# Kernel optimization log

Measured on AMD Instinct MI355X. Metric: run time of the kernel, lower is better.

## Reference

```python
import jax, jax.numpy as jnp
import numpy as np

D_IN = 1024
D_OUT = 1024
NUM_HEADS = 16
HEAD_DIM = D_OUT // NUM_HEADS


def setup_inputs() -> dict:
    key = jax.random.key(0)
    ks = jax.random.split(key, 9)
    s = 0.02
    return {
        "x": jax.random.normal(ks[0], (2, 2048, D_IN), dtype=jnp.float32),
        "Wq": jax.random.normal(ks[1], (D_IN, D_OUT), dtype=jnp.float32) * s,
        "bq": jnp.zeros((D_OUT,), dtype=jnp.float32),
        "Wk": jax.random.normal(ks[2], (D_IN, D_OUT), dtype=jnp.float32) * s,
        "bk": jnp.zeros((D_OUT,), dtype=jnp.float32),
        "Wv": jax.random.normal(ks[3], (D_IN, D_OUT), dtype=jnp.float32) * s,
        "bv": jnp.zeros((D_OUT,), dtype=jnp.float32),
        "Wo": jax.random.normal(ks[4], (D_OUT, D_OUT), dtype=jnp.float32) * s,
        "bo": jnp.zeros((D_OUT,), dtype=jnp.float32),
    }


def reference(x, Wq, bq, Wk, bk, Wv, bv, Wo, bo):
    B, S, _ = x.shape
    H, Dh = NUM_HEADS, HEAD_DIM
    q = (x @ Wq + bq).reshape(B, S, H, Dh).transpose(0, 2, 1, 3)  # bhsd
    k = (x @ Wk + bk).reshape(B, S, H, Dh).transpose(0, 2, 1, 3)
    v = (x @ Wv + bv).reshape(B, S, H, Dh).transpose(0, 2, 1, 3)
    scores = jnp.einsum("bhqd,bhkd->bhqk", q, k) * (Dh ** -0.5)
    causal = jnp.tril(jnp.ones((S, S), dtype=bool))
    scores = jnp.where(causal, scores, jnp.float32(-jnp.inf))
    w = jax.nn.softmax(scores, axis=-1)
    ctx = jnp.einsum("bhqk,bhkd->bhqd", w, v)
    ctx = ctx.transpose(0, 2, 1, 3).reshape(B, S, H * Dh)
    return ctx @ Wo + bo
```

## Files before the change

### kernel.cpp

```cpp
#include <hip/hip_runtime.h>
#include <cmath>

#define D_IN 1024
#define D_OUT 1024
#define NUM_HEADS 16
#define HEAD_DIM 64
#define BATCH 2
#define SEQ 2048
#define GK 1024
#define KT 32

typedef __attribute__((ext_vector_type(8))) short short8;
typedef __attribute__((ext_vector_type(4))) short short4v;
typedef __attribute__((ext_vector_type(4))) float float4v;

__device__ __forceinline__ unsigned short f2bf(float f) {
  unsigned int u = __builtin_bit_cast(unsigned int, f);
  unsigned int r = (u + 0x7FFFu + ((u >> 16) & 1u)) >> 16;
  return (unsigned short)r;
}
__device__ __forceinline__ float bf2f(unsigned short h) {
  return __builtin_bit_cast(float, (unsigned int)h << 16);
}

__device__ __forceinline__ void async_copy16(void* lds, const void* g) {
  __builtin_amdgcn_global_load_lds(
      (const __attribute__((address_space(1))) unsigned int*)g,
      (__attribute__((address_space(3))) unsigned int*)lds, 16, 0, 0);
}

#define DPP_F(x, ctrl) __builtin_bit_cast(float,                         \
    __builtin_amdgcn_update_dpp(__builtin_bit_cast(int, (x)),            \
                                __builtin_bit_cast(int, (x)),            \
                                (ctrl), 0xF, 0xF, false))

__device__ __forceinline__ float red16_sum(float x) {
  x += DPP_F(x, 0xB1);
  x += DPP_F(x, 0x4E);
  x += DPP_F(x, 0x124);
  x += DPP_F(x, 0x128);
  return x;
}

__global__ __launch_bounds__(256) void prep(
    const float* __restrict__ x, const float* __restrict__ Wq,
    const float* __restrict__ Wk, const float* __restrict__ Wv,
    const float* __restrict__ Wo, unsigned short* __restrict__ xb,
    unsigned short* __restrict__ wqkv_t, unsigned short* __restrict__ wo_t) {
  const int z = blockIdx.z;
  if (z == 4) {
    const int bid = blockIdx.y * 32 + blockIdx.x;
    const size_t i0 = ((size_t)bid * 256 + threadIdx.x) * 16;
#pragma unroll
    for (int half = 0; half < 2; ++half) {
      const size_t o = i0 + half * 8;
      float4 a = *(const float4*)(x + o);
      float4 b = *(const float4*)(x + o + 4);
      union { unsigned short u[8]; short8 v; } t;
      t.u[0] = f2bf(a.x); t.u[1] = f2bf(a.y); t.u[2] = f2bf(a.z); t.u[3] = f2bf(a.w);
      t.u[4] = f2bf(b.x); t.u[5] = f2bf(b.y); t.u[6] = f2bf(b.z); t.u[7] = f2bf(b.w);
      *(short8*)(xb + o) = t.v;
    }
    return;
  }
  const float* W = (z == 0) ? Wq : (z == 1) ? Wk : (z == 2) ? Wv : Wo;
  unsigned short* out = (z < 3) ? (wqkv_t + (size_t)z * 1024 * 1024) : wo_t;

  __shared__ float T[32][33];
  const int r = threadIdx.x >> 3;
  const int c4 = (threadIdx.x & 7) << 2;
  const int k0 = blockIdx.x * 32, n0 = blockIdx.y * 32;

  float4 v = *(const float4*)(W + (size_t)(k0 + r) * 1024 + n0 + c4);
  T[r][c4 + 0] = v.x; T[r][c4 + 1] = v.y; T[r][c4 + 2] = v.z; T[r][c4 + 3] = v.w;
  __syncthreads();

  union { unsigned short u[4]; short4v v4; } o;
#pragma unroll
  for (int i = 0; i < 4; ++i) o.u[i] = f2bf(T[c4 + i][r]);
  *(short4v*)(out + (size_t)(n0 + r) * 1024 + k0 + c4) = o.v4;
}

__device__ __forceinline__ void gemm_core(
    const unsigned short* __restrict__ A, const unsigned short* __restrict__ Bt,
    unsigned short* As, unsigned short* Bs, int bm, int bn, float4v acc[4][4]) {
  const int tid = threadIdx.x;
  const int wave = tid >> 6, lane = tid & 63;
  const int quad = lane >> 4, l16 = lane & 15;
  const int wr = wave >> 1, wc = wave & 1;
  const int sw = l16 & 7;

  int srow[4], sgc[4];
#pragma unroll
  for (int t = 0; t < 4; ++t) {
    const int c = (wave * 4 + t) * 64 + lane;
    srow[t] = c >> 3;
    sgc[t] = ((c & 7) ^ (srow[t] & 7)) * 8;
  }

  for (int k0 = 0; k0 < GK; k0 += 64) {
    __syncthreads();
#pragma unroll
    for (int t = 0; t < 4; ++t) {
      const int c = (wave * 4 + t) * 64 + lane;
      async_copy16(As + (size_t)c * 8, A + (size_t)(bm + srow[t]) * GK + k0 + sgc[t]);
    }
#pragma unroll
    for (int t = 0; t < 4; ++t) {
      const int c = (wave * 4 + t) * 64 + lane;
      async_copy16(Bs + (size_t)c * 8, Bt + (size_t)(bn + srow[t]) * GK + k0 + sgc[t]);
    }
    __syncthreads();

#pragma unroll
    for (int h = 0; h < 2; ++h) {
      short8 af[4], bf[4];
#pragma unroll
      for (int i = 0; i < 4; ++i) {
        const int row = wr * 64 + i * 16 + l16;
        af[i] = *(const short8*)&As[((size_t)row * 8 + ((h * 4 + quad) ^ sw)) * 8];
      }
#pragma unroll
      for (int j = 0; j < 4; ++j) {
        const int row = wc * 64 + j * 16 + l16;
        bf[j] = *(const short8*)&Bs[((size_t)row * 8 + ((h * 4 + quad) ^ sw)) * 8];
      }
#pragma unroll
      for (int i = 0; i < 4; ++i)
#pragma unroll
        for (int j = 0; j < 4; ++j)
          acc[i][j] = __builtin_amdgcn_mfma_f32_16x16x32_bf16(af[i], bf[j], acc[i][j], 0, 0, 0);
    }
  }
}

__global__ __launch_bounds__(256) void gemm_qkv(
    const unsigned short* __restrict__ A, const unsigned short* __restrict__ Bt,
    const float* __restrict__ bq, const float* __restrict__ bk,
    const float* __restrict__ bv,
    unsigned short* __restrict__ qbuf, unsigned short* __restrict__ kblk,
    unsigned short* __restrict__ vblk) {
  __shared__ unsigned short As[128 * 64];
  __shared__ unsigned short Bs[128 * 64];
  const int wave = threadIdx.x >> 6, lane = threadIdx.x & 63;
  const int quad = lane >> 4, l16 = lane & 15;
  const int wr = wave >> 1, wc = wave & 1;
  const int bm = blockIdx.x * 128, bn = blockIdx.y * 128;

  float4v acc[4][4] = {};
  gemm_core(A, Bt, As, Bs, bm, bn, acc);

#pragma unroll
  for (int j = 0; j < 4; ++j) {
    const int n = bn + wc * 64 + j * 16 + l16;
    const int seg = n >> 10, nn = n & 1023;
    const int h = nn >> 6, d = nn & 63;
    const float bsv = (seg == 0) ? bq[nn] : (seg == 1) ? bk[nn] : bv[nn];
    const float scale = (seg == 0) ? 0.18033688011112043f : 1.0f;
#pragma unroll
    for (int i = 0; i < 4; ++i) {
#pragma unroll
      for (int r = 0; r < 4; ++r) {
        const int m = bm + wr * 64 + i * 16 + quad * 4 + r;
        const int b = m >> 11, s = m & 2047;
        const int bh = b * NUM_HEADS + h;
        const unsigned short hv = f2bf((acc[i][j][r] + bsv) * scale);
        if (seg == 0) {
          qbuf[((size_t)bh * SEQ + s) * HEAD_DIM + d] = hv;
        } else if (seg == 1) {
          kblk[((size_t)bh * 64 + (s >> 5)) * 2048 +
               (size_t)(((((s >> 4) & 1) * 2 + (d >> 5)) * 64 +
                         ((d >> 3) & 3) * 16 + (s & 15)) * 8 + (d & 7))] = hv;
        } else {
          vblk[((size_t)bh * 64 + (s >> 5)) * 2048 +
               (size_t)(((d >> 4) * 64 + ((s >> 3) & 3) * 16 + (d & 15)) * 8 +
                        (s & 7))] = hv;
        }
      }
    }
  }
}

__global__ __launch_bounds__(256) void gemm_out(
    const unsigned short* __restrict__ A, const unsigned short* __restrict__ Bt,
    const float* __restrict__ bo, float* __restrict__ out) {
  __shared__ unsigned short As[128 * 64];
  __shared__ unsigned short Bs[128 * 64];
  const int wave = threadIdx.x >> 6, lane = threadIdx.x & 63;
  const int quad = lane >> 4, l16 = lane & 15;
  const int wr = wave >> 1, wc = wave & 1;
  const int bm = blockIdx.x * 128, bn = blockIdx.y * 128;

  float4v acc[4][4] = {};
  gemm_core(A, Bt, As, Bs, bm, bn, acc);

#pragma unroll
  for (int j = 0; j < 4; ++j) {
    const int n = bn + wc * 64 + j * 16 + l16;
    const float bsv = bo[n];
#pragma unroll
    for (int i = 0; i < 4; ++i) {
#pragma unroll
      for (int r = 0; r < 4; ++r) {
        const int m = bm + wr * 64 + i * 16 + quad * 4 + r;
        out[(size_t)m * D_OUT + n] = acc[i][j][r] + bsv;
      }
    }
  }
}

#define OBS 72

__global__ __launch_bounds__(256) void attn_kernel(
    const unsigned short* __restrict__ qf, const unsigned short* __restrict__ kblk,
    const unsigned short* __restrict__ vblk, unsigned short* __restrict__ ctx) {
  __shared__ unsigned short PL[4 * 32 * 40];
  __shared__ unsigned short OB[4 * 32 * OBS];
  __shared__ float LL[4 * 32];

  const int id = blockIdx.x;
  const int bh = id & 31;
  const int qblk = 63 - (id >> 5);
  const int qw0 = qblk * 32;
  const int tid = threadIdx.x;
  const int w = tid >> 6;
  const int lane = tid & 63;
  const int quad = lane >> 4;
  const int l16 = lane & 15;

  const int nt = qblk + 1;
  const int qch = (nt + 3) >> 2;
  const int t0 = w * qch;
  const int t1 = min(nt, t0 + qch);

  const size_t bh_base = (size_t)bh * SEQ * HEAD_DIM;
  const unsigned short* kb = kblk + bh_base;
  const unsigned short* vb = vblk + bh_base;

  short8 aq[2][2];
#pragma unroll
  for (int qt = 0; qt < 2; ++qt) {
    const unsigned short* qrow =
        qf + bh_base + (size_t)(qw0 + qt * 16 + l16) * HEAD_DIM + quad * 8;
    aq[qt][0] = *(const short8*)qrow;
    aq[qt][1] = *(const short8*)(qrow + 32);
  }

  float4v O[2][4] = {};
  float l_part[2][4] = {};
  unsigned short* PLw = PL + w * (32 * 40);

  if (t0 < t1) {
    short8 kA[4], vA[4], kB[4], vB[4];

    auto load = [&](int kt, short8 kd[4], short8 vd[4]) {
      const size_t base = (size_t)kt * 2048 + lane * 8;
#pragma unroll
      for (int f = 0; f < 4; ++f) kd[f] = *(const short8*)(kb + base + f * 512);
#pragma unroll
      for (int f = 0; f < 4; ++f) vd[f] = *(const short8*)(vb + base + f * 512);
    };

    auto step = [&](int kt, const short8 kd[4], const short8 vd[4], bool masked) {
      const int k0 = kt * KT;
      float4v cs[2][2];
#pragma unroll
      for (int qt = 0; qt < 2; ++qt)
#pragma unroll
        for (int g = 0; g < 2; ++g) {
          float4v c = {0.f, 0.f, 0.f, 0.f};
          c = __builtin_amdgcn_mfma_f32_16x16x32_bf16(aq[qt][0], kd[2 * g], c, 0, 0, 0);
          c = __builtin_amdgcn_mfma_f32_16x16x32_bf16(aq[qt][1], kd[2 * g + 1], c, 0, 0, 0);
          cs[qt][g] = c;
        }

#pragma unroll
      for (int qt = 0; qt < 2; ++qt)
#pragma unroll
        for (int g = 0; g < 2; ++g)
#pragma unroll
          for (int r = 0; r < 4; ++r) {
            float s = cs[qt][g][r];
            if (masked) {
              const int key = k0 + g * 16 + l16;
              const int qg = qw0 + qt * 16 + quad * 4 + r;
              s = (key <= qg) ? s : -1e30f;
            }
            const float p = __builtin_exp2f(s);
            l_part[qt][r] += p;
            const unsigned int pu = __builtin_bit_cast(unsigned int, p);
            PLw[(qt * 16 + quad * 4 + r) * 40 + (g * 2 + (l16 >> 3)) * 8 + (l16 & 7)] =
                (unsigned short)(pu >> 16);
          }

#pragma unroll
      for (int qt = 0; qt < 2; ++qt) {
        const short8 pA = *(const short8*)&PLw[(qt * 16 + l16) * 40 + quad * 8];
#pragma unroll
        for (int jj = 0; jj < 4; ++jj)
          O[qt][jj] = __builtin_amdgcn_mfma_f32_16x16x32_bf16(pA, vd[jj], O[qt][jj], 0, 0, 0);
      }
    };

    load(t0, kA, vA);
    int kt = t0;
    while (true) {
      const bool lastA = (kt == t1 - 1);
      if (!lastA) load(kt + 1, kB, vB);
      step(kt, kA, vA, kt == nt - 1);
      if (lastA) break;
      ++kt;
      const bool lastB = (kt == t1 - 1);
      if (!lastB) load(kt + 1, kA, vA);
      step(kt, kB, vB, kt == nt - 1);
      if (lastB) break;
      ++kt;
    }
  }

#pragma unroll
  for (int qt = 0; qt < 2; ++qt)
#pragma unroll
    for (int r = 0; r < 4; ++r) {
      const float lsum = red16_sum(l_part[qt][r]);
      const int row = qt * 16 + quad * 4 + r;
      if (l16 == 0) LL[w * 32 + row] = lsum;
#pragma unroll
      for (int jj = 0; jj < 4; ++jj)
        OB[(w * 32 + row) * OBS + jj * 16 + l16] = f2bf(O[qt][jj][r]);
    }

  __syncthreads();

  const int row = w * 8 + (lane >> 3);
  const int col0 = (lane & 7) * 8;
  float acc[8] = {};
#pragma unroll
  for (int u = 0; u < 4; ++u) {
    const short8 t = *(const short8*)&OB[(u * 32 + row) * OBS + col0];
#pragma unroll
    for (int i = 0; i < 8; ++i) acc[i] += bf2f((unsigned short)t[i]);
  }
  const float inv = 1.0f / (LL[row] + LL[32 + row] + LL[64 + row] + LL[96 + row]);
  union { unsigned short u[8]; short8 v; } o;
#pragma unroll
  for (int i = 0; i < 8; ++i) o.u[i] = f2bf(acc[i] * inv);
  const int b = bh >> 4, h = bh & 15;
  const int qg = qw0 + row;
  *(short8*)(ctx + ((size_t)b * SEQ + qg) * D_OUT + h * HEAD_DIM + col0) = o.v;
}

extern "C" void kernel_launch(void* const* d_in, const int* in_sizes, int n_in,
                              void* d_out, int out_size, void* d_ws, size_t ws_size,
                              hipStream_t stream) {
  const float* x  = (const float*)d_in[0];
  const float* Wq = (const float*)d_in[1];
  const float* bq = (const float*)d_in[2];
  const float* Wk = (const float*)d_in[3];
  const float* bk = (const float*)d_in[4];
  const float* Wv = (const float*)d_in[5];
  const float* bv = (const float*)d_in[6];
  const float* Wo = (const float*)d_in[7];
  const float* bo = (const float*)d_in[8];
  float* out = (float*)d_out;

  const int M = BATCH * SEQ;
  unsigned short* xb     = (unsigned short*)d_ws;
  unsigned short* wqkv_t = xb + (size_t)M * D_IN;
  unsigned short* wo_t   = wqkv_t + (size_t)3 * D_OUT * D_IN;
  unsigned short* qb     = wo_t + (size_t)D_OUT * D_OUT;
  unsigned short* kblk   = qb + (size_t)M * D_OUT;
  unsigned short* vblk   = kblk + (size_t)M * D_OUT;
  unsigned short* cb     = vblk + (size_t)M * D_OUT;

  prep<<<dim3(32, 32, 5), 256, 0, stream>>>(x, Wq, Wk, Wv, Wo, xb, wqkv_t, wo_t);
  gemm_qkv<<<dim3(M / 128, 3 * D_OUT / 128), 256, 0, stream>>>(
      xb, wqkv_t, bq, bk, bv, qb, kblk, vblk);
  attn_kernel<<<dim3(32 * 64), 256, 0, stream>>>(qb, kblk, vblk, cb);
  gemm_out<<<dim3(M / 128, D_OUT / 128), 256, 0, stream>>>(cb, wo_t, bo, out);
}
```

Baseline: 205.5 us.

## Software-pipeline attention PV with row sums via MFMA; shrink out-GEMM M tile

The attention inner loop is restructured so the P·V MFMAs for the previous key tile are issued after the current tile's QK^T MFMAs. A double-buffered P staging area and separate K/V prefetches overlap the softmax exp work with matrix math. Row sums of P now come from an extra MFMA against a vector of ones, replacing per-lane accumulation and the DPP reduction; this sums the bf16-rounded P, which slightly changes the numerics. The output projection GEMM is templated to a 64-row M tile, doubling its block count to improve occupancy and wave balance on the 1024-wide output.

```diff
diff --git a/kernel.cpp b/kernel.cpp
--- a/kernel.cpp
+++ b/kernel.cpp
@@ -27,19 +27,6 @@
   __builtin_amdgcn_global_load_lds(
       (const __attribute__((address_space(1))) unsigned int*)g,
       (__attribute__((address_space(3))) unsigned int*)lds, 16, 0, 0);
-}
-
-#define DPP_F(x, ctrl) __builtin_bit_cast(float,                         \
-    __builtin_amdgcn_update_dpp(__builtin_bit_cast(int, (x)),            \
-                                __builtin_bit_cast(int, (x)),            \
-                                (ctrl), 0xF, 0xF, false))
-
-__device__ __forceinline__ float red16_sum(float x) {
-  x += DPP_F(x, 0xB1);
-  x += DPP_F(x, 0x4E);
-  x += DPP_F(x, 0x124);
-  x += DPP_F(x, 0x128);
-  return x;
 }
 
 __global__ __launch_bounds__(256) void prep(
@@ -81,43 +68,53 @@
   *(short4v*)(out + (size_t)(n0 + r) * 1024 + k0 + c4) = o.v4;
 }
 
+template <int BMI>
 __device__ __forceinline__ void gemm_core(
     const unsigned short* __restrict__ A, const unsigned short* __restrict__ Bt,
-    unsigned short* As, unsigned short* Bs, int bm, int bn, float4v acc[4][4]) {
+    unsigned short* As, unsigned short* Bs, int bm, int bn,
+    float4v (&acc)[BMI / 32][4]) {
+  constexpr int MI = BMI / 32;
   const int tid = threadIdx.x;
   const int wave = tid >> 6, lane = tid & 63;
   const int quad = lane >> 4, l16 = lane & 15;
   const int wr = wave >> 1, wc = wave & 1;
   const int sw = l16 & 7;
 
-  int srow[4], sgc[4];
+  int srowA[MI], sgcA[MI];
+#pragma unroll
+  for (int t = 0; t < MI; ++t) {
+    const int c = (wave * MI + t) * 64 + lane;
+    srowA[t] = c >> 3;
+    sgcA[t] = ((c & 7) ^ (srowA[t] & 7)) * 8;
+  }
+  int srowB[4], sgcB[4];
 #pragma unroll
   for (int t = 0; t < 4; ++t) {
     const int c = (wave * 4 + t) * 64 + lane;
-    srow[t] = c >> 3;
-    sgc[t] = ((c & 7) ^ (srow[t] & 7)) * 8;
+    srowB[t] = c >> 3;
+    sgcB[t] = ((c & 7) ^ (srowB[t] & 7)) * 8;
   }
 
   for (int k0 = 0; k0 < GK; k0 += 64) {
     __syncthreads();
 #pragma unroll
+    for (int t = 0; t < MI; ++t) {
+      const int c = (wave * MI + t) * 64 + lane;
+      async_copy16(As + (size_t)c * 8, A + (size_t)(bm + srowA[t]) * GK + k0 + sgcA[t]);
+    }
+#pragma unroll
     for (int t = 0; t < 4; ++t) {
       const int c = (wave * 4 + t) * 64 + lane;
-      async_copy16(As + (size_t)c * 8, A + (size_t)(bm + srow[t]) * GK + k0 + sgc[t]);
-    }
-#pragma unroll
-    for (int t = 0; t < 4; ++t) {
-      const int c = (wave * 4 + t) * 64 + lane;
-      async_copy16(Bs + (size_t)c * 8, Bt + (size_t)(bn + srow[t]) * GK + k0 + sgc[t]);
+      async_copy16(Bs + (size_t)c * 8, Bt + (size_t)(bn + srowB[t]) * GK + k0 + sgcB[t]);
     }
     __syncthreads();
 
 #pragma unroll
     for (int h = 0; h < 2; ++h) {
-      short8 af[4], bf[4];
-#pragma unroll
-      for (int i = 0; i < 4; ++i) {
-        const int row = wr * 64 + i * 16 + l16;
+      short8 af[MI], bf[4];
+#pragma unroll
+      for (int i = 0; i < MI; ++i) {
+        const int row = wr * (BMI / 2) + i * 16 + l16;
         af[i] = *(const short8*)&As[((size_t)row * 8 + ((h * 4 + quad) ^ sw)) * 8];
       }
 #pragma unroll
@@ -126,7 +123,7 @@
         bf[j] = *(const short8*)&Bs[((size_t)row * 8 + ((h * 4 + quad) ^ sw)) * 8];
       }
 #pragma unroll
-      for (int i = 0; i < 4; ++i)
+      for (int i = 0; i < MI; ++i)
 #pragma unroll
         for (int j = 0; j < 4; ++j)
           acc[i][j] = __builtin_amdgcn_mfma_f32_16x16x32_bf16(af[i], bf[j], acc[i][j], 0, 0, 0);
@@ -148,7 +145,7 @@
   const int bm = blockIdx.x * 128, bn = blockIdx.y * 128;
 
   float4v acc[4][4] = {};
-  gemm_core(A, Bt, As, Bs, bm, bn, acc);
+  gemm_core<128>(A, Bt, As, Bs, bm, bn, acc);
 
 #pragma unroll
   for (int j = 0; j < 4; ++j) {
@@ -184,25 +181,25 @@
 __global__ __launch_bounds__(256) void gemm_out(
     const unsigned short* __restrict__ A, const unsigned short* __restrict__ Bt,
     const float* __restrict__ bo, float* __restrict__ out) {
-  __shared__ unsigned short As[128 * 64];
+  __shared__ unsigned short As[64 * 64];
   __shared__ unsigned short Bs[128 * 64];
   const int wave = threadIdx.x >> 6, lane = threadIdx.x & 63;
   const int quad = lane >> 4, l16 = lane & 15;
   const int wr = wave >> 1, wc = wave & 1;
-  const int bm = blockIdx.x * 128, bn = blockIdx.y * 128;
-
-  float4v acc[4][4] = {};
-  gemm_core(A, Bt, As, Bs, bm, bn, acc);
+  const int bm = blockIdx.x * 64, bn = blockIdx.y * 128;
+
+  float4v acc[2][4] = {};
+  gemm_core<64>(A, Bt, As, Bs, bm, bn, acc);
 
 #pragma unroll
   for (int j = 0; j < 4; ++j) {
     const int n = bn + wc * 64 + j * 16 + l16;
     const float bsv = bo[n];
 #pragma unroll
-    for (int i = 0; i < 4; ++i) {
+    for (int i = 0; i < 2; ++i) {
 #pragma unroll
       for (int r = 0; r < 4; ++r) {
-        const int m = bm + wr * 64 + i * 16 + quad * 4 + r;
+        const int m = bm + wr * 32 + i * 16 + quad * 4 + r;
         out[(size_t)m * D_OUT + n] = acc[i][j][r] + bsv;
       }
     }
@@ -214,7 +211,7 @@
 __global__ __launch_bounds__(256) void attn_kernel(
     const unsigned short* __restrict__ qf, const unsigned short* __restrict__ kblk,
     const unsigned short* __restrict__ vblk, unsigned short* __restrict__ ctx) {
-  __shared__ unsigned short PL[4 * 32 * 40];
+  __shared__ unsigned short PL[4 * 2 * 32 * 40];
   __shared__ unsigned short OB[4 * 32 * OBS];
   __shared__ float LL[4 * 32];
 
@@ -247,33 +244,59 @@
   }
 
   float4v O[2][4] = {};
-  float l_part[2][4] = {};
-  unsigned short* PLw = PL + w * (32 * 40);
+  float4v Ol[2] = {};
+  short8 pPrev[2];
+
+  union { unsigned short u[8]; short8 v; } onesu;
+#pragma unroll
+  for (int i = 0; i < 8; ++i) onesu.u[i] = 0x3F80;
+  const short8 onesf = onesu.v;
+
+  unsigned short* PLw = PL + w * (2 * 32 * 40);
 
   if (t0 < t1) {
-    short8 kA[4], vA[4], kB[4], vB[4];
-
-    auto load = [&](int kt, short8 kd[4], short8 vd[4]) {
+    short8 kf[4], vf[4];
+
+    auto loadK = [&](int kt) {
       const size_t base = (size_t)kt * 2048 + lane * 8;
 #pragma unroll
-      for (int f = 0; f < 4; ++f) kd[f] = *(const short8*)(kb + base + f * 512);
-#pragma unroll
-      for (int f = 0; f < 4; ++f) vd[f] = *(const short8*)(vb + base + f * 512);
+      for (int f = 0; f < 4; ++f) kf[f] = *(const short8*)(kb + base + f * 512);
     };
-
-    auto step = [&](int kt, const short8 kd[4], const short8 vd[4], bool masked) {
-      const int k0 = kt * KT;
+    auto loadV = [&](int kt) {
+      const size_t base = (size_t)kt * 2048 + lane * 8;
+#pragma unroll
+      for (int f = 0; f < 4; ++f) vf[f] = *(const short8*)(vb + base + f * 512);
+    };
+
+    loadK(t0);
+    for (int kt = t0; kt < t1; ++kt) {
       float4v cs[2][2];
 #pragma unroll
       for (int qt = 0; qt < 2; ++qt)
 #pragma unroll
         for (int g = 0; g < 2; ++g) {
           float4v c = {0.f, 0.f, 0.f, 0.f};
-          c = __builtin_amdgcn_mfma_f32_16x16x32_bf16(aq[qt][0], kd[2 * g], c, 0, 0, 0);
-          c = __builtin_amdgcn_mfma_f32_16x16x32_bf16(aq[qt][1], kd[2 * g + 1], c, 0, 0, 0);
+          c = __builtin_amdgcn_mfma_f32_16x16x32_bf16(aq[qt][0], kf[2 * g], c, 0, 0, 0);
+          c = __builtin_amdgcn_mfma_f32_16x16x32_bf16(aq[qt][1], kf[2 * g + 1], c, 0, 0, 0);
           cs[qt][g] = c;
         }
 
+      if (kt > t0) {
+#pragma unroll
+        for (int qt = 0; qt < 2; ++qt) {
+#pragma unroll
+          for (int jj = 0; jj < 4; ++jj)
+            O[qt][jj] = __builtin_amdgcn_mfma_f32_16x16x32_bf16(pPrev[qt], vf[jj], O[qt][jj], 0, 0, 0);
+          Ol[qt] = __builtin_amdgcn_mfma_f32_16x16x32_bf16(pPrev[qt], onesf, Ol[qt], 0, 0, 0);
+        }
+      }
+
+      if (kt + 1 < t1) loadK(kt + 1);
+      loadV(kt);
+
+      unsigned short* PLp = PLw + (kt & 1) * (32 * 40);
+      const bool masked = (kt == nt - 1);
+      const int k0 = kt * KT;
 #pragma unroll
       for (int qt = 0; qt < 2; ++qt)
 #pragma unroll
@@ -287,34 +310,22 @@
               s = (key <= qg) ? s : -1e30f;
             }
             const float p = __builtin_exp2f(s);
-            l_part[qt][r] += p;
             const unsigned int pu = __builtin_bit_cast(unsigned int, p);
-            PLw[(qt * 16 + quad * 4 + r) * 40 + (g * 2 + (l16 >> 3)) * 8 + (l16 & 7)] =
+            PLp[(qt * 16 + quad * 4 + r) * 40 + (g * 2 + (l16 >> 3)) * 8 + (l16 & 7)] =
                 (unsigned short)(pu >> 16);
           }
 
 #pragma unroll
-      for (int qt = 0; qt < 2; ++qt) {
-        const short8 pA = *(const short8*)&PLw[(qt * 16 + l16) * 40 + quad * 8];
-#pragma unroll
-        for (int jj = 0; jj < 4; ++jj)
-          O[qt][jj] = __builtin_amdgcn_mfma_f32_16x16x32_bf16(pA, vd[jj], O[qt][jj], 0, 0, 0);
-      }
-    };
-
-    load(t0, kA, vA);
-    int kt = t0;
-    while (true) {
-      const bool lastA = (kt == t1 - 1);
-      if (!lastA) load(kt + 1, kB, vB);
-      step(kt, kA, vA, kt == nt - 1);
-      if (lastA) break;
-      ++kt;
-      const bool lastB = (kt == t1 - 1);
-      if (!lastB) load(kt + 1, kA, vA);
-      step(kt, kB, vB, kt == nt - 1);
-      if (lastB) break;
-      ++kt;
+      for (int qt = 0; qt < 2; ++qt)
+        pPrev[qt] = *(const short8*)&PLp[(qt * 16 + l16) * 40 + quad * 8];
+    }
+
+#pragma unroll
+    for (int qt = 0; qt < 2; ++qt) {
+#pragma unroll
+      for (int jj = 0; jj < 4; ++jj)
+        O[qt][jj] = __builtin_amdgcn_mfma_f32_16x16x32_bf16(pPrev[qt], vf[jj], O[qt][jj], 0, 0, 0);
+      Ol[qt] = __builtin_amdgcn_mfma_f32_16x16x32_bf16(pPrev[qt], onesf, Ol[qt], 0, 0, 0);
     }
   }
 
@@ -322,9 +333,8 @@
   for (int qt = 0; qt < 2; ++qt)
 #pragma unroll
     for (int r = 0; r < 4; ++r) {
-      const float lsum = red16_sum(l_part[qt][r]);
       const int row = qt * 16 + quad * 4 + r;
-      if (l16 == 0) LL[w * 32 + row] = lsum;
+      if (l16 == 0) LL[w * 32 + row] = Ol[qt][r];
 #pragma unroll
       for (int jj = 0; jj < 4; ++jj)
         OB[(w * 32 + row) * OBS + jj * 16 + l16] = f2bf(O[qt][jj][r]);
@@ -377,5 +387,5 @@
   gemm_qkv<<<dim3(M / 128, 3 * D_OUT / 128), 256, 0, stream>>>(
       xb, wqkv_t, bq, bk, bv, qb, kblk, vblk);
   attn_kernel<<<dim3(32 * 64), 256, 0, stream>>>(qb, kblk, vblk, cb);
-  gemm_out<<<dim3(M / 128, D_OUT / 128), 256, 0, stream>>>(cb, wo_t, bo, out);
-}
+  gemm_out<<<dim3(M / 64, D_OUT / 128), 256, 0, stream>>>(cb, wo_t, bo, out);
+}
```

After: 206.5 us. Within noise of the previous version (+0.5%).

## Fuse all stages into one persistent cooperative kernel with atomic work queues

Applied to the files above, without the earlier changes.

Replaces the four separate launches (prep, QKV GEMM, attention, output GEMM) with a single persistent cooperative kernel that uses grid.sync between stages and atomic counters to hand out tiles dynamically. The output GEMM switches to 64-row tiles so it yields more tiles for better load balance. The aim is to cut launch gaps and stage-tail idle time, at the cost of grid-wide barriers, atomics, a memset, and an occupancy query on every call. If the cooperative launch fails, it falls back to four separate kernels.

```diff
diff --git a/kernel.cpp b/kernel.cpp
--- a/kernel.cpp
+++ b/kernel.cpp
@@ -1,5 +1,8 @@
 #include <hip/hip_runtime.h>
+#include <hip/hip_cooperative_groups.h>
 #include <cmath>
+
+namespace cg = cooperative_groups;
 
 #define D_IN 1024
 #define D_OUT 1024
@@ -9,6 +12,8 @@
 #define SEQ 2048
 #define GK 1024
 #define KT 32
+#define MAXGRID 768
+#define OBS 72
 
 typedef __attribute__((ext_vector_type(8))) short short8;
 typedef __attribute__((ext_vector_type(4))) short short4v;
@@ -42,82 +47,92 @@
   return x;
 }
 
-__global__ __launch_bounds__(256) void prep(
-    const float* __restrict__ x, const float* __restrict__ Wq,
+
+__device__ __forceinline__ void do_prep_job(
+    int job, char* SM, const float* __restrict__ x, const float* __restrict__ Wq,
     const float* __restrict__ Wk, const float* __restrict__ Wv,
     const float* __restrict__ Wo, unsigned short* __restrict__ xb,
     unsigned short* __restrict__ wqkv_t, unsigned short* __restrict__ wo_t) {
-  const int z = blockIdx.z;
+  const int tid = threadIdx.x;
+  const int z = job >> 10;
+  const int t = job & 1023;
   if (z == 4) {
-    const int bid = blockIdx.y * 32 + blockIdx.x;
-    const size_t i0 = ((size_t)bid * 256 + threadIdx.x) * 16;
+    const size_t i0 = ((size_t)t * 256 + tid) * 16;
 #pragma unroll
     for (int half = 0; half < 2; ++half) {
       const size_t o = i0 + half * 8;
       float4 a = *(const float4*)(x + o);
       float4 b = *(const float4*)(x + o + 4);
-      union { unsigned short u[8]; short8 v; } t;
-      t.u[0] = f2bf(a.x); t.u[1] = f2bf(a.y); t.u[2] = f2bf(a.z); t.u[3] = f2bf(a.w);
-      t.u[4] = f2bf(b.x); t.u[5] = f2bf(b.y); t.u[6] = f2bf(b.z); t.u[7] = f2bf(b.w);
-      *(short8*)(xb + o) = t.v;
+      union { unsigned short u[8]; short8 v; } tt;
+      tt.u[0] = f2bf(a.x); tt.u[1] = f2bf(a.y); tt.u[2] = f2bf(a.z); tt.u[3] = f2bf(a.w);
+      tt.u[4] = f2bf(b.x); tt.u[5] = f2bf(b.y); tt.u[6] = f2bf(b.z); tt.u[7] = f2bf(b.w);
+      *(short8*)(xb + o) = tt.v;
     }
     return;
   }
   const float* W = (z == 0) ? Wq : (z == 1) ? Wk : (z == 2) ? Wv : Wo;
-  unsigned short* out = (z < 3) ? (wqkv_t + (size_t)z * 1024 * 1024) : wo_t;
-
-  __shared__ float T[32][33];
-  const int r = threadIdx.x >> 3;
-  const int c4 = (threadIdx.x & 7) << 2;
-  const int k0 = blockIdx.x * 32, n0 = blockIdx.y * 32;
-
+  unsigned short* outp = (z < 3) ? (wqkv_t + (size_t)z * 1024 * 1024) : wo_t;
+  float (*T)[33] = (float(*)[33])SM;
+  const int r = tid >> 3;
+  const int c4 = (tid & 7) << 2;
+  const int k0 = (t & 31) * 32, n0 = (t >> 5) * 32;
+  __syncthreads();
   float4 v = *(const float4*)(W + (size_t)(k0 + r) * 1024 + n0 + c4);
   T[r][c4 + 0] = v.x; T[r][c4 + 1] = v.y; T[r][c4 + 2] = v.z; T[r][c4 + 3] = v.w;
   __syncthreads();
-
   union { unsigned short u[4]; short4v v4; } o;
 #pragma unroll
   for (int i = 0; i < 4; ++i) o.u[i] = f2bf(T[c4 + i][r]);
-  *(short4v*)(out + (size_t)(n0 + r) * 1024 + k0 + c4) = o.v4;
-}
-
+  *(short4v*)(outp + (size_t)(n0 + r) * 1024 + k0 + c4) = o.v4;
+}
+
+template <int BMI>
 __device__ __forceinline__ void gemm_core(
     const unsigned short* __restrict__ A, const unsigned short* __restrict__ Bt,
-    unsigned short* As, unsigned short* Bs, int bm, int bn, float4v acc[4][4]) {
+    unsigned short* As, unsigned short* Bs, int bm, int bn,
+    float4v (&acc)[BMI / 32][4]) {
+  constexpr int MI = BMI / 32;
   const int tid = threadIdx.x;
   const int wave = tid >> 6, lane = tid & 63;
   const int quad = lane >> 4, l16 = lane & 15;
   const int wr = wave >> 1, wc = wave & 1;
   const int sw = l16 & 7;
 
-  int srow[4], sgc[4];
+  int srowA[MI], sgcA[MI];
+#pragma unroll
+  for (int t = 0; t < MI; ++t) {
+    const int c = (wave * MI + t) * 64 + lane;
+    srowA[t] = c >> 3;
+    sgcA[t] = ((c & 7) ^ (srowA[t] & 7)) * 8;
+  }
+  int srowB[4], sgcB[4];
 #pragma unroll
   for (int t = 0; t < 4; ++t) {
     const int c = (wave * 4 + t) * 64 + lane;
-    srow[t] = c >> 3;
-    sgc[t] = ((c & 7) ^ (srow[t] & 7)) * 8;
+    srowB[t] = c >> 3;
+    sgcB[t] = ((c & 7) ^ (srowB[t] & 7)) * 8;
   }
 
   for (int k0 = 0; k0 < GK; k0 += 64) {
     __syncthreads();
+#pragma unroll
+    for (int t = 0; t < MI; ++t) {
+      const int c = (wave * MI + t) * 64 + lane;
+      async_copy16(As + (size_t)c * 8, A + (size_t)(bm + srowA[t]) * GK + k0 + sgcA[t]);
+    }
 #pragma unroll
     for (int t = 0; t < 4; ++t) {
       const int c = (wave * 4 + t) * 64 + lane;
-      async_copy16(As + (size_t)c * 8, A + (size_t)(bm + srow[t]) * GK + k0 + sgc[t]);
-    }
-#pragma unroll
-    for (int t = 0; t < 4; ++t) {
-      const int c = (wave * 4 + t) * 64 + lane;
-      async_copy16(Bs + (size_t)c * 8, Bt + (size_t)(bn + srow[t]) * GK + k0 + sgc[t]);
+      async_copy16(Bs + (size_t)c * 8, Bt + (size_t)(bn + srowB[t]) * GK + k0 + sgcB[t]);
     }
     __syncthreads();
 
 #pragma unroll
     for (int h = 0; h < 2; ++h) {
-      short8 af[4], bf[4];
-#pragma unroll
-      for (int i = 0; i < 4; ++i) {
-        const int row = wr * 64 + i * 16 + l16;
+      short8 af[MI], bf[4];
+#pragma unroll
+      for (int i = 0; i < MI; ++i) {
+        const int row = wr * (BMI / 2) + i * 16 + l16;
         af[i] = *(const short8*)&As[((size_t)row * 8 + ((h * 4 + quad) ^ sw)) * 8];
       }
 #pragma unroll
@@ -126,7 +141,7 @@
         bf[j] = *(const short8*)&Bs[((size_t)row * 8 + ((h * 4 + quad) ^ sw)) * 8];
       }
 #pragma unroll
-      for (int i = 0; i < 4; ++i)
+      for (int i = 0; i < MI; ++i)
 #pragma unroll
         for (int j = 0; j < 4; ++j)
           acc[i][j] = __builtin_amdgcn_mfma_f32_16x16x32_bf16(af[i], bf[j], acc[i][j], 0, 0, 0);
@@ -134,21 +149,22 @@
   }
 }
 
-__global__ __launch_bounds__(256) void gemm_qkv(
-    const unsigned short* __restrict__ A, const unsigned short* __restrict__ Bt,
-    const float* __restrict__ bq, const float* __restrict__ bk,
-    const float* __restrict__ bv,
+__device__ __forceinline__ void do_qkv_tile(
+    int tile, char* SM, const unsigned short* __restrict__ xb,
+    const unsigned short* __restrict__ wqkv_t, const float* __restrict__ bq,
+    const float* __restrict__ bk, const float* __restrict__ bv,
     unsigned short* __restrict__ qbuf, unsigned short* __restrict__ kblk,
     unsigned short* __restrict__ vblk) {
-  __shared__ unsigned short As[128 * 64];
-  __shared__ unsigned short Bs[128 * 64];
-  const int wave = threadIdx.x >> 6, lane = threadIdx.x & 63;
+  unsigned short* As = (unsigned short*)SM;
+  unsigned short* Bs = As + 8192;
+  const int tid = threadIdx.x;
+  const int wave = tid >> 6, lane = tid & 63;
   const int quad = lane >> 4, l16 = lane & 15;
   const int wr = wave >> 1, wc = wave & 1;
-  const int bm = blockIdx.x * 128, bn = blockIdx.y * 128;
+  const int bm = (tile & 31) * 128, bn = (tile >> 5) * 128;
 
   float4v acc[4][4] = {};
-  gemm_core(A, Bt, As, Bs, bm, bn, acc);
+  gemm_core<128>(xb, wqkv_t, As, Bs, bm, bn, acc);
 
 #pragma unroll
   for (int j = 0; j < 4; ++j) {
@@ -181,53 +197,24 @@
   }
 }
 
-__global__ __launch_bounds__(256) void gemm_out(
-    const unsigned short* __restrict__ A, const unsigned short* __restrict__ Bt,
-    const float* __restrict__ bo, float* __restrict__ out) {
-  __shared__ unsigned short As[128 * 64];
-  __shared__ unsigned short Bs[128 * 64];
-  const int wave = threadIdx.x >> 6, lane = threadIdx.x & 63;
-  const int quad = lane >> 4, l16 = lane & 15;
-  const int wr = wave >> 1, wc = wave & 1;
-  const int bm = blockIdx.x * 128, bn = blockIdx.y * 128;
-
-  float4v acc[4][4] = {};
-  gemm_core(A, Bt, As, Bs, bm, bn, acc);
-
-#pragma unroll
-  for (int j = 0; j < 4; ++j) {
-    const int n = bn + wc * 64 + j * 16 + l16;
-    const float bsv = bo[n];
-#pragma unroll
-    for (int i = 0; i < 4; ++i) {
-#pragma unroll
-      for (int r = 0; r < 4; ++r) {
-        const int m = bm + wr * 64 + i * 16 + quad * 4 + r;
-        out[(size_t)m * D_OUT + n] = acc[i][j][r] + bsv;
-      }
-    }
-  }
-}
-
-#define OBS 72
-
-__global__ __launch_bounds__(256) void attn_kernel(
-    const unsigned short* __restrict__ qf, const unsigned short* __restrict__ kblk,
-    const unsigned short* __restrict__ vblk, unsigned short* __restrict__ ctx) {
-  __shared__ unsigned short PL[4 * 32 * 40];
-  __shared__ unsigned short OB[4 * 32 * OBS];
-  __shared__ float LL[4 * 32];
-
-  const int id = blockIdx.x;
-  const int bh = id & 31;
-  const int qblk = 63 - (id >> 5);
-  const int qw0 = qblk * 32;
+__device__ __forceinline__ void do_attn_job(
+    int job, char* SM, const unsigned short* __restrict__ qbuf,
+    const unsigned short* __restrict__ kblk, const unsigned short* __restrict__ vblk,
+    unsigned short* __restrict__ cb) {
+  unsigned short* PL = (unsigned short*)SM;
+  unsigned short* OB = PL + 5120;
+  float* LL = (float*)(SM + 28672);
+
   const int tid = threadIdx.x;
   const int w = tid >> 6;
   const int lane = tid & 63;
   const int quad = lane >> 4;
   const int l16 = lane & 15;
 
+  const int bh = job & 31;
+  const int qblk = 63 - (job >> 5);
+  const int qw0 = qblk * 32;
+
   const int nt = qblk + 1;
   const int qch = (nt + 3) >> 2;
   const int t0 = w * qch;
@@ -236,19 +223,19 @@
   const size_t bh_base = (size_t)bh * SEQ * HEAD_DIM;
   const unsigned short* kb = kblk + bh_base;
   const unsigned short* vb = vblk + bh_base;
+  unsigned short* PLw = PL + w * (32 * 40);
 
   short8 aq[2][2];
 #pragma unroll
   for (int qt = 0; qt < 2; ++qt) {
     const unsigned short* qrow =
-        qf + bh_base + (size_t)(qw0 + qt * 16 + l16) * HEAD_DIM + quad * 8;
+        qbuf + bh_base + (size_t)(qw0 + qt * 16 + l16) * HEAD_DIM + quad * 8;
     aq[qt][0] = *(const short8*)qrow;
     aq[qt][1] = *(const short8*)(qrow + 32);
   }
 
   float4v O[2][4] = {};
   float l_part[2][4] = {};
-  unsigned short* PLw = PL + w * (32 * 40);
 
   if (t0 < t1) {
     short8 kA[4], vA[4], kB[4], vB[4];
@@ -347,7 +334,120 @@
   for (int i = 0; i < 8; ++i) o.u[i] = f2bf(acc[i] * inv);
   const int b = bh >> 4, h = bh & 15;
   const int qg = qw0 + row;
-  *(short8*)(ctx + ((size_t)b * SEQ + qg) * D_OUT + h * HEAD_DIM + col0) = o.v;
+  *(short8*)(cb + ((size_t)b * SEQ + qg) * D_OUT + h * HEAD_DIM + col0) = o.v;
+}
+
+__device__ __forceinline__ void do_out_tile(
+    int tile, char* SM, const unsigned short* __restrict__ cb,
+    const unsigned short* __restrict__ wo_t, const float* __restrict__ bo,
+    float* __restrict__ out) {
+  unsigned short* As = (unsigned short*)SM;
+  unsigned short* Bs = As + 4096;
+  const int tid = threadIdx.x;
+  const int wave = tid >> 6, lane = tid & 63;
+  const int quad = lane >> 4, l16 = lane & 15;
+  const int wr = wave >> 1, wc = wave & 1;
+  const int bm = (tile & 63) * 64, bn = (tile >> 6) * 128;
+
+  float4v acc[2][4] = {};
+  gemm_core<64>(cb, wo_t, As, Bs, bm, bn, acc);
+
+#pragma unroll
+  for (int j = 0; j < 4; ++j) {
+    const int n = bn + wc * 64 + j * 16 + l16;
+    const float bsv = bo[n];
+#pragma unroll
+    for (int i = 0; i < 2; ++i) {
+#pragma unroll
+      for (int r = 0; r < 4; ++r) {
+        const int m = bm + wr * 32 + i * 16 + quad * 4 + r;
+        out[(size_t)m * D_OUT + n] = acc[i][j][r] + bsv;
+      }
+    }
+  }
+}
+
+__global__ __launch_bounds__(256, 3) void fused(
+    const float* __restrict__ x, const float* __restrict__ Wq,
+    const float* __restrict__ Wk, const float* __restrict__ Wv,
+    const float* __restrict__ Wo, const float* __restrict__ bq,
+    const float* __restrict__ bk, const float* __restrict__ bv,
+    const float* __restrict__ bo, unsigned short* __restrict__ xb,
+    unsigned short* __restrict__ wqkv_t, unsigned short* __restrict__ wo_t,
+    unsigned short* __restrict__ qbuf, unsigned short* __restrict__ kblk,
+    unsigned short* __restrict__ vblk, unsigned short* __restrict__ cb,
+    float* __restrict__ out, unsigned int* __restrict__ counters) {
+  __shared__ __align__(16) char SM[32800];
+  cg::grid_group grid = cg::this_grid();
+  const int tid = threadIdx.x;
+  int* jobshare = (int*)(SM + 32768);
+
+  for (int job = blockIdx.x; job < 5120; job += gridDim.x)
+    do_prep_job(job, SM, x, Wq, Wk, Wv, Wo, xb, wqkv_t, wo_t);
+
+  grid.sync();
+
+  while (true) {
+    __syncthreads();
+    if (tid == 0) *jobshare = (int)atomicAdd(&counters[0], 1u);
+    __syncthreads();
+    const int tile = *jobshare;
+    if (tile >= 768) break;
+    do_qkv_tile(tile, SM, xb, wqkv_t, bq, bk, bv, qbuf, kblk, vblk);
+  }
+
+  grid.sync();
+
+  while (true) {
+    __syncthreads();
+    if (tid == 0) *jobshare = (int)atomicAdd(&counters[1], 1u);
+    __syncthreads();
+    const int job = *jobshare;
+    if (job >= 2048) break;
+    do_attn_job(job, SM, qbuf, kblk, vblk, cb);
+  }
+
+  grid.sync();
+
+  while (true) {
+    __syncthreads();
+    if (tid == 0) *jobshare = (int)atomicAdd(&counters[2], 1u);
+    __syncthreads();
+    const int tile = *jobshare;
+    if (tile >= 512) break;
+    do_out_tile(tile, SM, cb, wo_t, bo, out);
+  }
+}
+
+__global__ __launch_bounds__(256) void prep_k(
+    const float* x, const float* Wq, const float* Wk, const float* Wv,
+    const float* Wo, unsigned short* xb, unsigned short* wqkv_t,
+    unsigned short* wo_t) {
+  __shared__ __align__(16) char SM[4224];
+  for (int job = blockIdx.x; job < 5120; job += gridDim.x)
+    do_prep_job(job, SM, x, Wq, Wk, Wv, Wo, xb, wqkv_t, wo_t);
+}
+
+__global__ __launch_bounds__(256) void qkv_k(
+    const unsigned short* xb, const unsigned short* wqkv_t, const float* bq,
+    const float* bk, const float* bv, unsigned short* qbuf,
+    unsigned short* kblk, unsigned short* vblk) {
+  __shared__ __align__(16) char SM[32768];
+  do_qkv_tile(blockIdx.x, SM, xb, wqkv_t, bq, bk, bv, qbuf, kblk, vblk);
+}
+
+__global__ __launch_bounds__(256) void attn_k(
+    const unsigned short* qbuf, const unsigned short* kblk,
+    const unsigned short* vblk, unsigned short* cb) {
+  __shared__ __align__(16) char SM[29184];
+  do_attn_job(blockIdx.x, SM, qbuf, kblk, vblk, cb);
+}
+
+__global__ __launch_bounds__(256) void out_k(
+    const unsigned short* cb, const unsigned short* wo_t, const float* bo,
+    float* out) {
+  __shared__ __align__(16) char SM[24576];
+  do_out_tile(blockIdx.x, SM, cb, wo_t, bo, out);
 }
 
 extern "C" void kernel_launch(void* const* d_in, const int* in_sizes, int n_in,
@@ -362,7 +462,7 @@
   const float* bv = (const float*)d_in[6];
   const float* Wo = (const float*)d_in[7];
   const float* bo = (const float*)d_in[8];
-  float* out = (float*)d_out;
+  float* outp = (float*)d_out;
 
   const int M = BATCH * SEQ;
   unsigned short* xb     = (unsigned short*)d_ws;
@@ -372,10 +472,27 @@
   unsigned short* kblk   = qb + (size_t)M * D_OUT;
   unsigned short* vblk   = kblk + (size_t)M * D_OUT;
   unsigned short* cb     = vblk + (size_t)M * D_OUT;
-
-  prep<<<dim3(32, 32, 5), 256, 0, stream>>>(x, Wq, Wk, Wv, Wo, xb, wqkv_t, wo_t);
-  gemm_qkv<<<dim3(M / 128, 3 * D_OUT / 128), 256, 0, stream>>>(
-      xb, wqkv_t, bq, bk, bv, qb, kblk, vblk);
-  attn_kernel<<<dim3(32 * 64), 256, 0, stream>>>(qb, kblk, vblk, cb);
-  gemm_out<<<dim3(M / 128, D_OUT / 128), 256, 0, stream>>>(cb, wo_t, bo, out);
-}
+  unsigned int*   counters = (unsigned int*)(cb + (size_t)M * D_OUT);
+
+  hipMemsetAsync(counters, 0, 16, stream);
+
+  int maxPerCU = 0;
+  hipError_t qerr = hipOccupancyMaxActiveBlocksPerMultiprocessor(
+      &maxPerCU, fused, 256, 0);
+  int grid = (qerr == hipSuccess) ? maxPerCU * 256 : 0;
+  if (grid > MAXGRID) grid = MAXGRID;
+
+  hipError_t err = hipErrorUnknown;
+  if (grid >= 256) {
+    void* args[] = {&x, &Wq, &Wk, &Wv, &Wo, &bq, &bk, &bv, &bo,
+                    &xb, &wqkv_t, &wo_t, &qb, &kblk, &vblk, &cb, &outp, &counters};
+    err = hipLaunchCooperativeKernel((const void*)fused, dim3(grid), dim3(256),
+                                     args, 0, stream);
+  }
+  if (err != hipSuccess) {
+    prep_k<<<768, 256, 0, stream>>>(x, Wq, Wk, Wv, Wo, xb, wqkv_t, wo_t);
+    qkv_k<<<768, 256, 0, stream>>>(xb, wqkv_t, bq, bk, bv, qb, kblk, vblk);
+    attn_k<<<2048, 256, 0, stream>>>(qb, kblk, vblk, cb);
+    out_k<<<512, 256, 0, stream>>>(cb, wo_t, bo, outp);
+  }
+}
```

Measured after the change: 407.8 us. 1.98x slower.
